# Kernel optimization log

Hardware: AMD Instinct MI355X
Metric: run time of the kernel (lower is better)

## Reference

```python
import jax, jax.numpy as jnp
import numpy as np

N_NODES = 100000
N_EDGES = 3200000
N_GRAPHS = 256
FEAT = 128
HIDDEN = 128
N_CLASSES = 10


def setup_inputs() -> dict:
    key = jax.random.key(0)
    ks = jax.random.split(key, 12)
    x = jax.random.normal(ks[0], (N_NODES, FEAT), dtype=jnp.float32)
    edge_index = jax.random.randint(ks[1], (2, N_EDGES), 0, N_NODES, dtype=jnp.int64)
    batch = jnp.sort(jax.random.randint(ks[2], (N_NODES,), 0, N_GRAPHS, dtype=jnp.int64))
    s = 0.05
    return {
        "x": x,
        "edge_index": edge_index,
        "batch": batch,
        "W1": jax.random.normal(ks[3], (FEAT, HIDDEN), dtype=jnp.float32) * s,
        "b1": jnp.zeros((HIDDEN,), dtype=jnp.float32),
        "W2": jax.random.normal(ks[4], (HIDDEN, HIDDEN), dtype=jnp.float32) * s,
        "b2": jnp.zeros((HIDDEN,), dtype=jnp.float32),
        "W3": jax.random.normal(ks[5], (HIDDEN, HIDDEN), dtype=jnp.float32) * s,
        "b3": jnp.zeros((HIDDEN,), dtype=jnp.float32),
        "lin1_w": jax.random.normal(ks[6], (HIDDEN, HIDDEN), dtype=jnp.float32) * s,
        "lin1_b": jnp.zeros((HIDDEN,), dtype=jnp.float32),
        "lin2_w": jax.random.normal(ks[7], (HIDDEN, N_CLASSES), dtype=jnp.float32) * s,
        "lin2_b": jnp.zeros((N_CLASSES,), dtype=jnp.float32),
    }


def _gcn_norm(edge_index, n_nodes):
    # PyG GCNConv default: add self-loops, symmetric normalization.
    src = jnp.concatenate([edge_index[0], jnp.arange(n_nodes, dtype=edge_index.dtype)])
    dst = jnp.concatenate([edge_index[1], jnp.arange(n_nodes, dtype=edge_index.dtype)])
    deg = jax.ops.segment_sum(jnp.ones_like(dst, dtype=jnp.float32), dst, num_segments=n_nodes)
    dis = jnp.where(deg > 0, jax.lax.rsqrt(jnp.maximum(deg, 1.0)), 0.0)
    norm = dis[src] * dis[dst]  # [E + N]
    return src, dst, norm


def _gcn_conv(x, src, dst, norm, W, b, n_nodes):
    h = x @ W                               # [N, H]
    msg = h[src] * norm[:, None]            # gather + scale, [E+N, H]
    out = jax.ops.segment_sum(msg, dst, num_segments=n_nodes)  # scatter-add
    return out + b


def reference(x, edge_index, batch, W1, b1, W2, b2, W3, b3, lin1_w, lin1_b, lin2_w, lin2_b):
    n = x.shape[0]
    src, dst, norm = _gcn_norm(edge_index, n)
    h = jax.nn.relu(_gcn_conv(x, src, dst, norm, W1, b1, n))
    h = jax.nn.relu(_gcn_conv(h, src, dst, norm, W2, b2, n))
    h = jax.nn.relu(_gcn_conv(h, src, dst, norm, W3, b3, n))
    # global mean pool over graphs
    sums = jax.ops.segment_sum(h, batch, num_segments=N_GRAPHS)
    cnts = jax.ops.segment_sum(jnp.ones((n,), dtype=h.dtype), batch, num_segments=N_GRAPHS)
    g = sums / jnp.maximum(cnts, 1.0)[:, None]
    g = jax.nn.relu(g @ lin1_w + lin1_b)
    # dropout p=0.5 is identity at inference
    return g @ lin2_w + lin2_b
```

## Files before the change

### kernel.cpp

```cpp
#include <hip/hip_runtime.h>
#include <hip/hip_fp16.h>

#define FEAT 128
#define CHUNK 8192
#define BSH 7
#define CAP 6144
#define RSTRIDE 784

#define QS  16.0f
#define QSI 0.0625f

typedef _Float16 half8 __attribute__((ext_vector_type(8)));
typedef float floatx4 __attribute__((ext_vector_type(4)));
typedef float floatx2 __attribute__((ext_vector_type(2)));

__device__ __forceinline__ floatx2 dec8(unsigned short q) {
  return __builtin_amdgcn_cvt_pk_f32_fp8((unsigned int)q, false);
}
__device__ __forceinline__ unsigned int enc8x4(float a, float b, float c, float d) {
  unsigned int r = __builtin_amdgcn_cvt_pk_fp8_f32(a, b, 0u, false);
  return __builtin_amdgcn_cvt_pk_fp8_f32(c, d, r, true);
}


__global__ __launch_bounds__(256) void sort_prep_kernel(
    const int* __restrict__ ei, int E, int nchunks, int nbuk,
    int* __restrict__ pairs, int* __restrict__ runs,
    const float* __restrict__ W1, const float* __restrict__ W2,
    const float* __restrict__ W3, _Float16* __restrict__ P1,
    _Float16* __restrict__ P2, _Float16* __restrict__ P3) {
  __shared__ int lhist[1024];
  __shared__ int lofs[1024];
  __shared__ int lcur[1024];
  __shared__ int tsum[256];
  __shared__ int stage[CHUNK];
  int t = threadIdx.x;
  if ((int)blockIdx.x >= nchunks) {
    int b = blockIdx.x - nchunks;
    const float* W = (b < 8) ? W1 : (b < 16) ? W2 : W3;
    _Float16* P = (b < 8) ? P1 : (b < 16) ? P2 : P3;
    int e = (b & 7) * 256 + t;
    int l = e & 63;
    int ks = (e >> 6) & 3;
    int tn = e >> 8;
    int n = tn * 16 + (l & 15);
    int k0 = ks * 32 + (l >> 4) * 8;
    half8 v;
#pragma unroll
    for (int j = 0; j < 8; ++j) v[j] = (_Float16)W[(k0 + j) * 128 + n];
    *(half8*)(P + (size_t)e * 8) = v;
    return;
  }
  int c = blockIdx.x;
  int e0 = c * CHUNK;
  int e1 = e0 + CHUNK; if (e1 > E) e1 = E;
  int cnt = e1 - e0;
#pragma unroll
  for (int u = 0; u < 4; ++u) lhist[t + u * 256] = 0;
  __syncthreads();
  for (int j = e0 + t; j < e1; j += 256) atomicAdd(&lhist[ei[E + j] >> BSH], 1);
  __syncthreads();
  int a0 = lhist[4 * t], a1 = lhist[4 * t + 1];
  int a2 = lhist[4 * t + 2], a3 = lhist[4 * t + 3];
  int s = ((a0 + a1) + (a2 + a3));
  tsum[t] = s;
  __syncthreads();
  for (int o = 1; o < 256; o <<= 1) {
    int x = (t >= o) ? tsum[t - o] : 0;
    __syncthreads();
    tsum[t] += x;
    __syncthreads();
  }
  int base = tsum[t] - s;
  lofs[4 * t] = base;       lcur[4 * t] = base;
  lofs[4 * t + 1] = base + a0;           lcur[4 * t + 1] = base + a0;
  lofs[4 * t + 2] = base + a0 + a1;      lcur[4 * t + 2] = base + a0 + a1;
  lofs[4 * t + 3] = base + a0 + a1 + a2; lcur[4 * t + 3] = base + a0 + a1 + a2;
  __syncthreads();
  for (int k = t; k < nbuk; k += 256) runs[(size_t)c * RSTRIDE + k] = lofs[k];
  if (t == 0) runs[(size_t)c * RSTRIDE + nbuk] = cnt;
  for (int j = e0 + t; j < e1; j += 256) {
    int sv = ei[j];
    int d = ei[E + j];
    int p = atomicAdd(&lcur[d >> BSH], 1);
    stage[p] = sv | ((d & 127) << 24);
  }
  __syncthreads();
  for (int j = t; j < cnt; j += 256) pairs[e0 + j] = stage[j];
}

__global__ __launch_bounds__(256) void bucket_csr_kernel(
    const int* __restrict__ pairs, const int* __restrict__ runs, int nchunks,
    int nbuk, int2* __restrict__ row_se, float* __restrict__ dis,
    int* __restrict__ col, int N) {
  __shared__ int rs[512], rl[512], ro[512];
  __shared__ int cnt[128], sc[128];
  __shared__ int stage[CAP];
  int b = blockIdx.x, t = threadIdx.x;
  for (int c = t; c < 512; c += 256) {
    int s0 = 0, len = 0;
    if (c < nchunks) {
      const int* rr = runs + (size_t)c * RSTRIDE;
      s0 = rr[b];
      len = rr[b + 1] - s0;
    }
    rs[c] = s0; rl[c] = len;
  }
  if (t < 128) cnt[t] = 0;
  __syncthreads();
  ro[t] = rl[t]; ro[t + 256] = rl[t + 256];
  __syncthreads();
  for (int o = 1; o < 512; o <<= 1) {
    int v0 = (t >= o) ? ro[t - o] : 0;
    int v1 = (t + 256 >= o) ? ro[t + 256 - o] : 0;
    __syncthreads();
    ro[t] += v0; ro[t + 256] += v1;
    __syncthreads();
  }
  int ce = ro[511];
  int y0 = ro[t] - rl[t];
  int y1 = ro[t + 256] - rl[t + 256];
  __syncthreads();
  ro[t] = y0; ro[t + 256] = y1;
  __syncthreads();
  int colbase = b * CAP;
  bool fits = ce <= CAP;
  if (fits) {
    for (int c = t; c < nchunks; c += 256) {
      int gs = c * CHUNK + rs[c];
      int base = ro[c];
      int len = rl[c];
      for (int j = 0; j < len; ++j) {
        int p = pairs[gs + j];
        stage[base + j] = p;
        atomicAdd(&cnt[((unsigned)p) >> 24], 1);
      }
    }
  } else {
    for (int c = t; c < nchunks; c += 256) {
      int gs = c * CHUNK + rs[c];
      for (int j = 0; j < rl[c]; ++j)
        atomicAdd(&cnt[((unsigned)pairs[gs + j]) >> 24], 1);
    }
  }
  __syncthreads();
  int v = 0, excl = 0;
  if (t < 128) { v = cnt[t]; sc[t] = v; }
  __syncthreads();
  for (int o = 1; o < 128; o <<= 1) {
    int x = (t >= o && t < 128) ? sc[t - o] : 0;
    __syncthreads();
    if (t < 128) sc[t] += x;
    __syncthreads();
  }
  if (t < 128) {
    excl = sc[t] - v;
    int node = b * 128 + t;
    if (node < N) {
      row_se[node] = make_int2(colbase + excl, colbase + excl + v);
      dis[node] = rsqrtf((float)(v + 1));
    }
    cnt[t] = excl;
  }
  __syncthreads();
  if (fits) {
    for (int j = t; j < ce; j += 256) {
      int p = stage[j];
      int loc = atomicAdd(&cnt[((unsigned)p) >> 24], 1);
      col[colbase + loc] = (p & 0xFFFFFF) << 7;
    }
  } else {
    for (int c = t; c < nchunks; c += 256) {
      int gs = c * CHUNK + rs[c];
      for (int j = 0; j < rl[c]; ++j) {
        int p = pairs[gs + j];
        int loc = atomicAdd(&cnt[((unsigned)p) >> 24], 1);
        if (loc < CAP) col[colbase + loc] = (p & 0xFFFFFF) << 7;
      }
    }
  }
}


__global__ __launch_bounds__(256) void mm1_kernel(
    const float* __restrict__ Av, const _Float16* __restrict__ Wpk,
    const float* __restrict__ scale, unsigned char* __restrict__ C, int N) {
  int t = threadIdx.x;
  int wave = t >> 6, lane = t & 63;
  int quad = lane >> 4, nidx = lane & 15;
  int m0 = blockIdx.x * 64 + wave * 16;
  int arow = m0 + nidx;
  bool avalid = arow < N;
  floatx4 acc[8];
#pragma unroll
  for (int tn = 0; tn < 8; ++tn) acc[tn] = (floatx4){0.f, 0.f, 0.f, 0.f};
#pragma unroll
  for (int ks = 0; ks < 4; ++ks) {
    half8 x = {};
    if (avalid) {
      const float* p = Av + (size_t)arow * 128 + ks * 32 + quad * 8;
      float4 f0 = *(const float4*)p;
      float4 f1 = *(const float4*)(p + 4);
      x[0] = (_Float16)f0.x; x[1] = (_Float16)f0.y;
      x[2] = (_Float16)f0.z; x[3] = (_Float16)f0.w;
      x[4] = (_Float16)f1.x; x[5] = (_Float16)f1.y;
      x[6] = (_Float16)f1.z; x[7] = (_Float16)f1.w;
    }
#pragma unroll
    for (int tn = 0; tn < 8; ++tn) {
      half8 wfrag = *(const half8*)(Wpk + ((size_t)((tn * 4 + ks) * 64 + lane)) * 8);
      acc[tn] = __builtin_amdgcn_mfma_f32_16x16x32_f16(wfrag, x, acc[tn], 0, 0, 0);
    }
  }
  if (avalid) {
    float s = scale[arow] * QS;
#pragma unroll
    for (int tn = 0; tn < 8; ++tn) {
      unsigned int r = enc8x4(acc[tn][0] * s, acc[tn][1] * s,
                              acc[tn][2] * s, acc[tn][3] * s);
      *(unsigned int*)(C + (size_t)arow * 128 + tn * 16 + quad * 4) = r;
    }
  }
}

__global__ __launch_bounds__(256) void agg_fuse_kernel(
    const unsigned char* __restrict__ hs_in, const int2* __restrict__ row_se,
    const int* __restrict__ col, const float* __restrict__ dis,
    const float* __restrict__ bias, const _Float16* __restrict__ Wpk,
    unsigned char* __restrict__ hs_out, int N) {
  __shared__ _Float16 Xs[16][136];
  int t = threadIdx.x;
  int wave = t >> 6, lane = t & 63;
  int n0 = blockIdx.x * 16;
  const char* hb = (const char*)hs_in + lane * 2;
  float2 b2 = ((const float2*)bias)[lane];
  for (int s = 0; s < 4; ++s) {
    int nl = wave * 4 + s;
    int node = n0 + nl;
    float ox = 0.f, oy = 0.f;
    if (node < N) {
      floatx2 sv = dec8(*(const unsigned short*)(hb + ((size_t)node << 7)));
      float ax = sv.x, ay = sv.y;
      int2 se = row_se[node];
      int i = se.x, e = se.y;
      for (; i + 16 <= e; i += 16) {
        unsigned short q[16];
#pragma unroll
        for (int u = 0; u < 16; ++u)
          q[u] = *(const unsigned short*)(hb + col[i + u]);
        float bx = 0.f, by = 0.f;
#pragma unroll
        for (int u = 0; u < 16; ++u) {
          floatx2 v = dec8(q[u]);
          bx += v.x; by += v.y;
        }
        ax += bx; ay += by;
      }
      for (; i + 4 <= e; i += 4) {
        floatx2 v0 = dec8(*(const unsigned short*)(hb + col[i + 0]));
        floatx2 v1 = dec8(*(const unsigned short*)(hb + col[i + 1]));
        floatx2 v2 = dec8(*(const unsigned short*)(hb + col[i + 2]));
        floatx2 v3 = dec8(*(const unsigned short*)(hb + col[i + 3]));
        ax += (v0.x + v1.x) + (v2.x + v3.x);
        ay += (v0.y + v1.y) + (v2.y + v3.y);
      }
      for (; i < e; ++i) {
        floatx2 v = dec8(*(const unsigned short*)(hb + col[i]));
        ax += v.x; ay += v.y;
      }
      float d = dis[node] * QSI;
      ox = fmaxf(fmaf(d, ax, b2.x), 0.f);
      oy = fmaxf(fmaf(d, ay, b2.y), 0.f);
    }
    *(__half2*)&Xs[nl][2 * lane] = __floats2half2_rn(ox, oy);
  }
  __syncthreads();
  int quad = lane >> 4, nidx = lane & 15;
  floatx4 acc0 = (floatx4){0.f, 0.f, 0.f, 0.f};
  floatx4 acc1 = (floatx4){0.f, 0.f, 0.f, 0.f};
  int tn0 = wave * 2;
#pragma unroll
  for (int ks = 0; ks < 4; ++ks) {
    half8 x = *(const half8*)&Xs[nidx][ks * 32 + quad * 8];
    half8 w0 = *(const half8*)(Wpk + ((size_t)((tn0 * 4 + ks) * 64 + lane)) * 8);
    half8 w1 = *(const half8*)(Wpk + ((size_t)(((tn0 + 1) * 4 + ks) * 64 + lane)) * 8);
    acc0 = __builtin_amdgcn_mfma_f32_16x16x32_f16(w0, x, acc0, 0, 0, 0);
    acc1 = __builtin_amdgcn_mfma_f32_16x16x32_f16(w1, x, acc1, 0, 0, 0);
  }
  int node = n0 + nidx;
  if (node < N) {
    float sc = dis[node] * QS;
    unsigned int r0 = enc8x4(acc0[0] * sc, acc0[1] * sc, acc0[2] * sc, acc0[3] * sc);
    *(unsigned int*)(hs_out + (size_t)node * 128 + tn0 * 16 + quad * 4) = r0;
    unsigned int r1 = enc8x4(acc1[0] * sc, acc1[1] * sc, acc1[2] * sc, acc1[3] * sc);
    *(unsigned int*)(hs_out + (size_t)node * 128 + (tn0 + 1) * 16 + quad * 4) = r1;
  }
}

__global__ __launch_bounds__(256) void agg_kernel(
    const unsigned char* __restrict__ hs, const int2* __restrict__ row_se,
    const int* __restrict__ col, const float* __restrict__ dis,
    const float* __restrict__ bias, __half* __restrict__ out, int N) {
  int node = blockIdx.x * 4 + (threadIdx.x >> 6);
  int lane = threadIdx.x & 63;
  if (node >= N) return;
  const char* hb = (const char*)hs + lane * 2;
  floatx2 sv = dec8(*(const unsigned short*)(hb + ((size_t)node << 7)));
  float ax = sv.x, ay = sv.y;
  int2 se = row_se[node];
  int i = se.x, e = se.y;
  for (; i + 16 <= e; i += 16) {
    unsigned short q[16];
#pragma unroll
    for (int u = 0; u < 16; ++u) q[u] = *(const unsigned short*)(hb + col[i + u]);
    float bx = 0.f, by = 0.f;
#pragma unroll
    for (int u = 0; u < 16; ++u) {
      floatx2 v = dec8(q[u]);
      bx += v.x; by += v.y;
    }
    ax += bx; ay += by;
  }
  for (; i + 4 <= e; i += 4) {
    floatx2 v0 = dec8(*(const unsigned short*)(hb + col[i + 0]));
    floatx2 v1 = dec8(*(const unsigned short*)(hb + col[i + 1]));
    floatx2 v2 = dec8(*(const unsigned short*)(hb + col[i + 2]));
    floatx2 v3 = dec8(*(const unsigned short*)(hb + col[i + 3]));
    ax += (v0.x + v1.x) + (v2.x + v3.x);
    ay += (v0.y + v1.y) + (v2.y + v3.y);
  }
  for (; i < e; ++i) {
    floatx2 v = dec8(*(const unsigned short*)(hb + col[i]));
    ax += v.x; ay += v.y;
  }
  float d = dis[node] * QSI;
  float2 b2 = ((const float2*)bias)[lane];
  float ox = fmaxf(fmaf(d, ax, b2.x), 0.f);
  float oy = fmaxf(fmaf(d, ay, b2.y), 0.f);
  ((__half2*)out)[(size_t)node * 64 + lane] = __floats2half2_rn(ox, oy);
}

__global__ __launch_bounds__(128) void head_kernel(
    const __half* __restrict__ h, const int* __restrict__ batch,
    const float* __restrict__ l1w, const float* __restrict__ l1b,
    const float* __restrict__ l2w, const float* __restrict__ l2b,
    float* __restrict__ out, int N, int C) {
  __shared__ float row[128];
  __shared__ float row2[128];
  int grp = blockIdx.x, t = threadIdx.x;
  int lo = 0, hi = N;
  while (lo < hi) { int m = (lo + hi) >> 1; if (batch[m] < grp) lo = m + 1; else hi = m; }
  int start = lo;
  hi = N;
  while (lo < hi) { int m = (lo + hi) >> 1; if (batch[m] <= grp) lo = m + 1; else hi = m; }
  int end = lo;
  float a0 = 0.f, a1 = 0.f, a2 = 0.f, a3 = 0.f;
  int i = start;
  for (; i + 4 <= end; i += 4) {
    a0 += __half2float(h[(size_t)i * 128 + t]);
    a1 += __half2float(h[(size_t)(i + 1) * 128 + t]);
    a2 += __half2float(h[(size_t)(i + 2) * 128 + t]);
    a3 += __half2float(h[(size_t)(i + 3) * 128 + t]);
  }
  for (; i < end; ++i) a0 += __half2float(h[(size_t)i * 128 + t]);
  float sum = (a0 + a1) + (a2 + a3);
  float cntf = (float)(end - start);
  row[t] = sum / fmaxf(cntf, 1.0f);
  __syncthreads();
  float acc = l1b[t];
#pragma unroll 8
  for (int k = 0; k < 128; ++k) acc = fmaf(row[k], l1w[k * 128 + t], acc);
  row2[t] = fmaxf(acc, 0.f);
  __syncthreads();
  if (t < C) {
    float a = l2b[t];
#pragma unroll 8
    for (int k = 0; k < 128; ++k) a = fmaf(row2[k], l2w[k * C + t], a);
    out[grp * C + t] = a;
  }
}


extern "C" void kernel_launch(void* const* d_in, const int* in_sizes, int n_in,
                              void* d_out, int out_size, void* d_ws, size_t ws_size,
                              hipStream_t stream) {
  const float* x   = (const float*)d_in[0];
  const int*   ei  = (const int*)d_in[1];
  const int*   bat = (const int*)d_in[2];
  const float* W1  = (const float*)d_in[3];
  const float* b1  = (const float*)d_in[4];
  const float* W2  = (const float*)d_in[5];
  const float* b2  = (const float*)d_in[6];
  const float* W3  = (const float*)d_in[7];
  const float* b3  = (const float*)d_in[8];
  const float* l1w = (const float*)d_in[9];
  const float* l1b = (const float*)d_in[10];
  const float* l2w = (const float*)d_in[11];
  const float* l2b = (const float*)d_in[12];

  int N = in_sizes[2];
  int E = in_sizes[1] / 2;
  int C = in_sizes[12];
  int G = out_size / C;
  float* outp = (float*)d_out;

  char* wp = (char*)d_ws;
  auto alloc = [&](size_t bytes) -> void* {
    void* p = (void*)wp;
    wp += (bytes + 255) & ~(size_t)255;
    return p;
  };
  int nbuk    = (N + 127) / 128;
  int nchunks = (E + CHUNK - 1) / CHUNK;

  float*    dis    = (float*)alloc((size_t)N * 4);
  int2*     row_se = (int2*)alloc((size_t)N * 8);
  int*      col    = (int*)alloc((size_t)nbuk * CAP * 4);
  int*      pairs  = (int*)alloc((size_t)nchunks * CHUNK * 4);
  int*      runs   = (int*)alloc((size_t)nchunks * RSTRIDE * 4);
  _Float16* Wpk1   = (_Float16*)alloc(16384 * 2);
  _Float16* Wpk2   = (_Float16*)alloc(16384 * 2);
  _Float16* Wpk3   = (_Float16*)alloc(16384 * 2);
  unsigned char* qA = (unsigned char*)alloc((size_t)N * FEAT);
  unsigned char* qB = (unsigned char*)alloc((size_t)N * FEAT);
  __half*   hout  = (__half*)alloc((size_t)N * FEAT * 2);

  sort_prep_kernel<<<nchunks + 24, 256, 0, stream>>>(
      ei, E, nchunks, nbuk, pairs, runs, W1, W2, W3, Wpk1, Wpk2, Wpk3);
  bucket_csr_kernel<<<nbuk, 256, 0, stream>>>(pairs, runs, nchunks, nbuk,
                                              row_se, dis, col, N);

  int mmB = (N + 63) / 64;
  int fB  = (N + 15) / 16;
  int agB = (N + 3) / 4;

  mm1_kernel<<<mmB, 256, 0, stream>>>(x, Wpk1, dis, qA, N);
  agg_fuse_kernel<<<fB, 256, 0, stream>>>(qA, row_se, col, dis, b1,
                                          Wpk2, qB, N);
  agg_fuse_kernel<<<fB, 256, 0, stream>>>(qB, row_se, col, dis, b2,
                                          Wpk3, qA, N);
  agg_kernel<<<agB, 256, 0, stream>>>(qA, row_se, col, dis, b3, hout, N);
  head_kernel<<<G, 128, 0, stream>>>(hout, bat, l1w, l1b, l2w, l2b, outp, N, C);
}
```

Baseline: 484.7 us.

## Aggregate neighbors with 16 lanes per node and 8-byte fp8 gathers

The aggregation kernels now assign 16 lanes per node, so one wave covers four nodes, and each lane gathers 8 fp8 features with a single 8-byte load instead of 2 bytes per lane across 64 lanes. The tail loops are replaced by a wave-uniform 16-wide unrolled loop. Out-of-range neighbors are redirected to an extra zeroed row appended to each feature buffer, which the prep kernel clears. This is meant to raise bytes per memory request and the number of gathers in flight. The cost is wasted loads when nodes in the same wave have different degrees.

```diff
diff --git a/kernel.cpp b/kernel.cpp
--- a/kernel.cpp
+++ b/kernel.cpp
@@ -14,12 +14,14 @@
 typedef float floatx4 __attribute__((ext_vector_type(4)));
 typedef float floatx2 __attribute__((ext_vector_type(2)));
 
-__device__ __forceinline__ floatx2 dec8(unsigned short q) {
-  return __builtin_amdgcn_cvt_pk_f32_fp8((unsigned int)q, false);
-}
 __device__ __forceinline__ unsigned int enc8x4(float a, float b, float c, float d) {
   unsigned int r = __builtin_amdgcn_cvt_pk_fp8_f32(a, b, 0u, false);
   return __builtin_amdgcn_cvt_pk_fp8_f32(c, d, r, true);
+}
+__device__ __forceinline__ void acc8(unsigned int w, float* a) {
+  floatx2 v0 = __builtin_amdgcn_cvt_pk_f32_fp8(w, false);
+  floatx2 v1 = __builtin_amdgcn_cvt_pk_f32_fp8(w, true);
+  a[0] += v0.x; a[1] += v0.y; a[2] += v1.x; a[3] += v1.y;
 }
 
 
@@ -28,7 +30,8 @@
     int* __restrict__ pairs, int* __restrict__ runs,
     const float* __restrict__ W1, const float* __restrict__ W2,
     const float* __restrict__ W3, _Float16* __restrict__ P1,
-    _Float16* __restrict__ P2, _Float16* __restrict__ P3) {
+    _Float16* __restrict__ P2, _Float16* __restrict__ P3,
+    unsigned char* __restrict__ qA, unsigned char* __restrict__ qB, int N) {
   __shared__ int lhist[1024];
   __shared__ int lofs[1024];
   __shared__ int lcur[1024];
@@ -37,6 +40,11 @@
   int t = threadIdx.x;
   if ((int)blockIdx.x >= nchunks) {
     int b = blockIdx.x - nchunks;
+    if (b == 24) {
+      if (t < 16) ((unsigned long long*)(qA + (size_t)N * FEAT))[t] = 0ull;
+      else if (t < 32) ((unsigned long long*)(qB + (size_t)N * FEAT))[t - 16] = 0ull;
+      return;
+    }
     const float* W = (b < 8) ? W1 : (b < 16) ? W2 : W3;
     _Float16* P = (b < 8) ? P1 : (b < 16) ? P2 : P3;
     int e = (b & 7) * 256 + t;
@@ -231,49 +239,37 @@
   __shared__ _Float16 Xs[16][136];
   int t = threadIdx.x;
   int wave = t >> 6, lane = t & 63;
-  int n0 = blockIdx.x * 16;
-  const char* hb = (const char*)hs_in + lane * 2;
-  float2 b2 = ((const float2*)bias)[lane];
-  for (int s = 0; s < 4; ++s) {
-    int nl = wave * 4 + s;
-    int node = n0 + nl;
-    float ox = 0.f, oy = 0.f;
-    if (node < N) {
-      floatx2 sv = dec8(*(const unsigned short*)(hb + ((size_t)node << 7)));
-      float ax = sv.x, ay = sv.y;
-      int2 se = row_se[node];
-      int i = se.x, e = se.y;
-      for (; i + 16 <= e; i += 16) {
-        unsigned short q[16];
-#pragma unroll
-        for (int u = 0; u < 16; ++u)
-          q[u] = *(const unsigned short*)(hb + col[i + u]);
-        float bx = 0.f, by = 0.f;
-#pragma unroll
-        for (int u = 0; u < 16; ++u) {
-          floatx2 v = dec8(q[u]);
-          bx += v.x; by += v.y;
-        }
-        ax += bx; ay += by;
-      }
-      for (; i + 4 <= e; i += 4) {
-        floatx2 v0 = dec8(*(const unsigned short*)(hb + col[i + 0]));
-        floatx2 v1 = dec8(*(const unsigned short*)(hb + col[i + 1]));
-        floatx2 v2 = dec8(*(const unsigned short*)(hb + col[i + 2]));
-        floatx2 v3 = dec8(*(const unsigned short*)(hb + col[i + 3]));
-        ax += (v0.x + v1.x) + (v2.x + v3.x);
-        ay += (v0.y + v1.y) + (v2.y + v3.y);
-      }
-      for (; i < e; ++i) {
-        floatx2 v = dec8(*(const unsigned short*)(hb + col[i]));
-        ax += v.x; ay += v.y;
-      }
-      float d = dis[node] * QSI;
-      ox = fmaxf(fmaf(d, ax, b2.x), 0.f);
-      oy = fmaxf(fmaf(d, ay, b2.y), 0.f);
-    }
-    *(__half2*)&Xs[nl][2 * lane] = __floats2half2_rn(ox, oy);
-  }
+  int lin = lane & 15;
+  int nl = wave * 4 + (lane >> 4);
+  int node = blockIdx.x * 16 + nl;
+  bool valid = node < N;
+  int lin8 = lin * 8;
+  int zoff = N << 7;
+  float a[8] = {0.f, 0.f, 0.f, 0.f, 0.f, 0.f, 0.f, 0.f};
+  int selfoff = (valid ? (node << 7) : zoff) + lin8;
+  uint2 s0 = *(const uint2*)(hs_in + (unsigned)selfoff);
+  acc8(s0.x, a); acc8(s0.y, a + 4);
+  int2 se = valid ? row_se[node] : make_int2(0, 0);
+  int i = se.x, e = se.y;
+  while (__any(i < e)) {
+#pragma unroll
+    for (int u = 0; u < 16; ++u) {
+      int idx = i + u;
+      int off = (idx < e) ? col[idx] : zoff;
+      uint2 r = *(const uint2*)(hs_in + (unsigned)(off + lin8));
+      acc8(r.x, a); acc8(r.y, a + 4);
+    }
+    i += 16;
+  }
+  float d = valid ? dis[node] * QSI : 0.f;
+  const float* bp = bias + lin8;
+  half8 hx;
+#pragma unroll
+  for (int j = 0; j < 8; ++j) {
+    float o = valid ? fmaxf(fmaf(d, a[j], bp[j]), 0.f) : 0.f;
+    hx[j] = (_Float16)o;
+  }
+  *(half8*)&Xs[nl][lin8] = hx;
   __syncthreads();
   int quad = lane >> 4, nidx = lane & 15;
   floatx4 acc0 = (floatx4){0.f, 0.f, 0.f, 0.f};
@@ -287,57 +283,53 @@
     acc0 = __builtin_amdgcn_mfma_f32_16x16x32_f16(w0, x, acc0, 0, 0, 0);
     acc1 = __builtin_amdgcn_mfma_f32_16x16x32_f16(w1, x, acc1, 0, 0, 0);
   }
-  int node = n0 + nidx;
-  if (node < N) {
-    float sc = dis[node] * QS;
+  int onode = blockIdx.x * 16 + nidx;
+  if (onode < N) {
+    float sc = dis[onode] * QS;
     unsigned int r0 = enc8x4(acc0[0] * sc, acc0[1] * sc, acc0[2] * sc, acc0[3] * sc);
-    *(unsigned int*)(hs_out + (size_t)node * 128 + tn0 * 16 + quad * 4) = r0;
+    *(unsigned int*)(hs_out + (size_t)onode * 128 + tn0 * 16 + quad * 4) = r0;
     unsigned int r1 = enc8x4(acc1[0] * sc, acc1[1] * sc, acc1[2] * sc, acc1[3] * sc);
-    *(unsigned int*)(hs_out + (size_t)node * 128 + (tn0 + 1) * 16 + quad * 4) = r1;
+    *(unsigned int*)(hs_out + (size_t)onode * 128 + (tn0 + 1) * 16 + quad * 4) = r1;
   }
 }
 
 __global__ __launch_bounds__(256) void agg_kernel(
     const unsigned char* __restrict__ hs, const int2* __restrict__ row_se,
     const int* __restrict__ col, const float* __restrict__ dis,
-    const float* __restrict__ bias, __half* __restrict__ out, int N) {
-  int node = blockIdx.x * 4 + (threadIdx.x >> 6);
-  int lane = threadIdx.x & 63;
-  if (node >= N) return;
-  const char* hb = (const char*)hs + lane * 2;
-  floatx2 sv = dec8(*(const unsigned short*)(hb + ((size_t)node << 7)));
-  float ax = sv.x, ay = sv.y;
-  int2 se = row_se[node];
+    const float* __restrict__ bias, _Float16* __restrict__ out, int N) {
+  int t = threadIdx.x;
+  int wave = t >> 6, lane = t & 63;
+  int lin = lane & 15;
+  int nl = wave * 4 + (lane >> 4);
+  int node = blockIdx.x * 16 + nl;
+  bool valid = node < N;
+  int lin8 = lin * 8;
+  int zoff = N << 7;
+  float a[8] = {0.f, 0.f, 0.f, 0.f, 0.f, 0.f, 0.f, 0.f};
+  int selfoff = (valid ? (node << 7) : zoff) + lin8;
+  uint2 s0 = *(const uint2*)(hs + (unsigned)selfoff);
+  acc8(s0.x, a); acc8(s0.y, a + 4);
+  int2 se = valid ? row_se[node] : make_int2(0, 0);
   int i = se.x, e = se.y;
-  for (; i + 16 <= e; i += 16) {
-    unsigned short q[16];
-#pragma unroll
-    for (int u = 0; u < 16; ++u) q[u] = *(const unsigned short*)(hb + col[i + u]);
-    float bx = 0.f, by = 0.f;
+  while (__any(i < e)) {
 #pragma unroll
     for (int u = 0; u < 16; ++u) {
-      floatx2 v = dec8(q[u]);
-      bx += v.x; by += v.y;
-    }
-    ax += bx; ay += by;
-  }
-  for (; i + 4 <= e; i += 4) {
-    floatx2 v0 = dec8(*(const unsigned short*)(hb + col[i + 0]));
-    floatx2 v1 = dec8(*(const unsigned short*)(hb + col[i + 1]));
-    floatx2 v2 = dec8(*(const unsigned short*)(hb + col[i + 2]));
-    floatx2 v3 = dec8(*(const unsigned short*)(hb + col[i + 3]));
-    ax += (v0.x + v1.x) + (v2.x + v3.x);
-    ay += (v0.y + v1.y) + (v2.y + v3.y);
-  }
-  for (; i < e; ++i) {
-    floatx2 v = dec8(*(const unsigned short*)(hb + col[i]));
-    ax += v.x; ay += v.y;
-  }
-  float d = dis[node] * QSI;
-  float2 b2 = ((const float2*)bias)[lane];
-  float ox = fmaxf(fmaf(d, ax, b2.x), 0.f);
-  float oy = fmaxf(fmaf(d, ay, b2.y), 0.f);
-  ((__half2*)out)[(size_t)node * 64 + lane] = __floats2half2_rn(ox, oy);
+      int idx = i + u;
+      int off = (idx < e) ? col[idx] : zoff;
+      uint2 r = *(const uint2*)(hs + (unsigned)(off + lin8));
+      acc8(r.x, a); acc8(r.y, a + 4);
+    }
+    i += 16;
+  }
+  if (valid) {
+    float d = dis[node] * QSI;
+    const float* bp = bias + lin8;
+    half8 hx;
+#pragma unroll
+    for (int j = 0; j < 8; ++j)
+      hx[j] = (_Float16)fmaxf(fmaf(d, a[j], bp[j]), 0.f);
+    *(half8*)(out + (size_t)node * FEAT + lin8) = hx;
+  }
 }
 
 __global__ __launch_bounds__(128) void head_kernel(
@@ -421,24 +413,25 @@
   _Float16* Wpk1   = (_Float16*)alloc(16384 * 2);
   _Float16* Wpk2   = (_Float16*)alloc(16384 * 2);
   _Float16* Wpk3   = (_Float16*)alloc(16384 * 2);
-  unsigned char* qA = (unsigned char*)alloc((size_t)N * FEAT);
-  unsigned char* qB = (unsigned char*)alloc((size_t)N * FEAT);
-  __half*   hout  = (__half*)alloc((size_t)N * FEAT * 2);
-
-  sort_prep_kernel<<<nchunks + 24, 256, 0, stream>>>(
-      ei, E, nchunks, nbuk, pairs, runs, W1, W2, W3, Wpk1, Wpk2, Wpk3);
+  unsigned char* qA = (unsigned char*)alloc((size_t)(N + 1) * FEAT);
+  unsigned char* qB = (unsigned char*)alloc((size_t)(N + 1) * FEAT);
+  _Float16* hout  = (_Float16*)alloc((size_t)N * FEAT * 2);
+
+  sort_prep_kernel<<<nchunks + 25, 256, 0, stream>>>(
+      ei, E, nchunks, nbuk, pairs, runs, W1, W2, W3, Wpk1, Wpk2, Wpk3,
+      qA, qB, N);
   bucket_csr_kernel<<<nbuk, 256, 0, stream>>>(pairs, runs, nchunks, nbuk,
                                               row_se, dis, col, N);
 
   int mmB = (N + 63) / 64;
   int fB  = (N + 15) / 16;
-  int agB = (N + 3) / 4;
 
   mm1_kernel<<<mmB, 256, 0, stream>>>(x, Wpk1, dis, qA, N);
   agg_fuse_kernel<<<fB, 256, 0, stream>>>(qA, row_se, col, dis, b1,
                                           Wpk2, qB, N);
   agg_fuse_kernel<<<fB, 256, 0, stream>>>(qB, row_se, col, dis, b2,
                                           Wpk3, qA, N);
-  agg_kernel<<<agB, 256, 0, stream>>>(qA, row_se, col, dis, b3, hout, N);
-  head_kernel<<<G, 128, 0, stream>>>(hout, bat, l1w, l1b, l2w, l2b, outp, N, C);
-}
+  agg_kernel<<<fB, 256, 0, stream>>>(qA, row_se, col, dis, b3, hout, N);
+  head_kernel<<<G, 128, 0, stream>>>((const __half*)hout, bat, l1w, l1b,
+                                     l2w, l2b, outp, N, C);
+}
```

Result: slower. 525.9 us (+8.5%).
